# Kernel optimization log

Measured on AMD Instinct MI355X. Metric: run time of the kernel, lower is better.

## Reference

```python
import jax, jax.numpy as jnp
import numpy as np

DIM = 768
HEADS = 12
HEAD_DIM = DIM // HEADS
SCALE = HEAD_DIM ** (-0.5)
BATCH = 1
SEQ = 4096


def setup_inputs() -> dict:
    key = jax.random.key(0)
    ks = jax.random.split(key, 5)
    x = jax.random.normal(ks[0], (BATCH, SEQ, DIM), dtype=jnp.float32)
    # Linear params stored (in, out) for y = x @ W + b
    w_qkv = jax.random.normal(ks[1], (DIM, 3 * DIM), dtype=jnp.float32) * (DIM ** -0.5)
    b_qkv = jnp.zeros((3 * DIM,), dtype=jnp.float32)
    w_proj = jax.random.normal(ks[2], (DIM, DIM), dtype=jnp.float32) * (DIM ** -0.5)
    b_proj = jnp.zeros((DIM,), dtype=jnp.float32)
    return {"x": x, "w_qkv": w_qkv, "b_qkv": b_qkv, "w_proj": w_proj, "b_proj": b_proj}


def reference(x, w_qkv, b_qkv, w_proj, b_proj):
    B, S, _ = x.shape
    qkv = x @ w_qkv + b_qkv                              # [B,S,3*DIM]
    qkv = qkv.reshape(B, S, 3, HEADS, HEAD_DIM)
    q, k, v = qkv[:, :, 0], qkv[:, :, 1], qkv[:, :, 2]   # [B,S,H,D]
    # scaled dot-product attention, full score matrix as in the original
    attn = jnp.einsum("bqhd,bkhd->bhqk", q * SCALE, k)   # [B,H,S,S]
    attn = jax.nn.softmax(attn, axis=-1)
    out = jnp.einsum("bhqk,bkhd->bqhd", attn, v)         # [B,S,H,D]
    out = out.reshape(B, S, DIM)
    return out @ w_proj + b_proj
```

## Files before the change

### kernel.cpp

```cpp
#include <hip/hip_runtime.h>
#include <hip/hip_bf16.h>

#define SEQ   4096
#define DIM   768
#define HEADS 12
#define NQKV  2304
#define QSCALE 0.18033688011f

#if __has_builtin(__builtin_amdgcn_exp2f)
#define EXP2(x) __builtin_amdgcn_exp2f(x)
#else
#define EXP2(x) __expf((x) * 0.69314718056f)
#endif

typedef __bf16 bf16_t;
typedef bf16_t bf16x8 __attribute__((ext_vector_type(8)));
typedef float  f32x4  __attribute__((ext_vector_type(4)));
typedef float  f32x16 __attribute__((ext_vector_type(16)));
typedef unsigned short u16;
typedef unsigned int   u32;

static __device__ __forceinline__ float bf2f(u16 v) {
    union { float f; unsigned u; } x; x.u = ((unsigned)v) << 16; return x.f;
}
static __device__ __forceinline__ u16 f2bf(float f) {
    union { float f; unsigned u; } x; x.f = f;
    unsigned r = x.u + 0x7fff + ((x.u >> 16) & 1);
    return (u16)(r >> 16);
}
static __device__ __forceinline__ u32 fbits(float f) {
    union { float f; unsigned u; } x; x.f = f; return x.u;
}
static __device__ __forceinline__ void gload_lds16(const u16* g, u16* l) {
    __builtin_amdgcn_global_load_lds(
        (const __attribute__((address_space(1))) unsigned int*)g,
        (__attribute__((address_space(3))) unsigned int*)l, 16, 0, 0);
}

static __device__ __forceinline__ int detect_f32(const u32* __restrict__ x) {
    int lane = threadIdx.x & 63;
    int cnt = 0;
#pragma unroll
    for (int i = 0; i < 8; ++i) {
        u32 w = x[lane * 8 + i];
        cnt += (((w >> 7) & 0xFF) >= 0x8F) ? 1 : 0;
    }
#pragma unroll
    for (int m = 1; m < 64; m <<= 1) cnt += __shfl_xor(cnt, m);
    return cnt >= 64;
}

__global__ __launch_bounds__(256) void prep(
    const void* __restrict__ x, const void* __restrict__ wqkv,
    const void* __restrict__ bqkv, const void* __restrict__ wproj,
    const void* __restrict__ bproj,
    u16* __restrict__ cvt, u16* __restrict__ wqkvT, u16* __restrict__ wprojT)
{
    __shared__ u16 tile[64][65];
    const bool f32 = detect_f32((const u32*)x) != 0;
    const int b = blockIdx.x;
    const int t = threadIdx.x;

    if (b < 576) {
        const void* src; u16* dst; int K, N, tx, ty;
        if (b < 432) { src = wqkv; dst = wqkvT; K = DIM; N = NQKV; tx = b % 36; ty = b / 36; }
        else { int bb = b - 432; src = wproj; dst = wprojT; K = DIM; N = DIM; tx = bb % 12; ty = bb / 12; }
        const int k0 = ty * 64, n0 = tx * 64;
#pragma unroll
        for (int i = 0; i < 16; ++i) {
            int idx = i * 256 + t;
            int r = idx >> 6, c = idx & 63;
            size_t si = (size_t)(k0 + r) * N + n0 + c;
            tile[r][c] = f32 ? f2bf(((const float*)src)[si]) : ((const u16*)src)[si];
        }
        __syncthreads();
#pragma unroll
        for (int i = 0; i < 16; ++i) {
            int idx = i * 256 + t;
            int r = idx >> 6, c = idx & 63;
            dst[(size_t)(n0 + r) * K + k0 + c] = tile[c][r];
        }
    } else {
        const int SX = SEQ * DIM, e1 = SX + NQKV;
        const int n_cvt = e1 + DIM;
        for (int i = (b - 576) * 256 + t; i < n_cvt; i += 200 * 256) {
            const void* s; int off;
            if      (i < SX) { s = x; off = i; }
            else if (i < e1) { s = bqkv; off = i - SX; }
            else             { s = bproj; off = i - e1; }
            cvt[i] = f32 ? f2bf(((const float*)s)[off]) : ((const u16*)s)[off];
        }
    }
}

template<int MODE>
__global__ __launch_bounds__(256) void gemm128(
    const u16* __restrict__ A, const u16* __restrict__ BT, const u16* __restrict__ bias,
    u16* __restrict__ C0, float* __restrict__ Cf, u16* __restrict__ VT,
    const u32* __restrict__ xdet, int M, int N, int K)
{
    __shared__ u16 a_lds[128 * 32];
    __shared__ u16 b_lds[128 * 32];

    const int t    = threadIdx.x;
    const int w    = t >> 6;
    const int lane = t & 63;
    const int l15  = lane & 15;
    const int quad = lane >> 4;
    const int wm   = w >> 1, wn = w & 1;
    const int m0   = blockIdx.y * 128, n0 = blockIdx.x * 128;

    const int srow = w * 32 + (lane >> 2);
    const int kch  = (lane & 3) * 8;
    const u16* asrc = A  + (size_t)(m0 + srow) * K + kch;
    const u16* bsrc = BT + (size_t)(n0 + srow) * K + kch;
    u16* adst = a_lds + w * 32 * 32;
    u16* bdst = b_lds + w * 32 * 32;

    f32x4 acc[4][4] = {};

    for (int kt = 0; kt < K; kt += 32) {
        __syncthreads();
        gload_lds16(asrc,          adst);
        gload_lds16(asrc + 16 * K, adst + 16 * 32);
        gload_lds16(bsrc,          bdst);
        gload_lds16(bsrc + 16 * K, bdst + 16 * 32);
        asrc += 32; bsrc += 32;
        __syncthreads();

        const u16* ab = a_lds + (wm * 64 + l15) * 32 + quad * 8;
        const u16* bb = b_lds + (wn * 64 + l15) * 32 + quad * 8;
        bf16x8 af[4], bfr[4];
#pragma unroll
        for (int i = 0; i < 4; ++i) af[i]  = *(const bf16x8*)(ab + i * 16 * 32);
#pragma unroll
        for (int j = 0; j < 4; ++j) bfr[j] = *(const bf16x8*)(bb + j * 16 * 32);
#pragma unroll
        for (int i = 0; i < 4; ++i)
#pragma unroll
            for (int j = 0; j < 4; ++j)
                acc[i][j] = __builtin_amdgcn_mfma_f32_16x16x32_bf16(af[i], bfr[j], acc[i][j], 0, 0, 0);
    }

    if constexpr (MODE == 1) {
        if (n0 >= 1536) {
            __shared__ u16 t_lds[128 * 136];
#pragma unroll
            for (int i = 0; i < 4; ++i)
#pragma unroll
                for (int j = 0; j < 4; ++j)
#pragma unroll
                    for (int r = 0; r < 4; ++r) {
                        int ml = wm * 64 + i * 16 + quad * 4 + r;
                        int nl = wn * 64 + j * 16 + l15;
                        int mpl = (ml & ~15) | (ml & 3) |
                                  (((ml >> 2) & 1) << 3) | (((ml >> 3) & 1) << 2);
                        float v = acc[i][j][r] + bf2f(bias[n0 + nl]);
                        t_lds[nl * 136 + mpl] = f2bf(v);
                    }
            __syncthreads();
            const int rr = t >> 4;
            const int mo = (t & 15) * 8;
#pragma unroll
            for (int it = 0; it < 8; ++it) {
                int nl = rr + it * 16;
                *(bf16x8*)(VT + (size_t)(n0 - 1536 + nl) * SEQ + m0 + mo) =
                    *(const bf16x8*)(t_lds + nl * 136 + mo);
            }
            return;
        }
    }

    bool outf32 = false;
    if (MODE == 0) outf32 = detect_f32(xdet) != 0;
#pragma unroll
    for (int i = 0; i < 4; ++i)
#pragma unroll
        for (int j = 0; j < 4; ++j)
#pragma unroll
            for (int r = 0; r < 4; ++r) {
                int m = m0 + wm * 64 + i * 16 + quad * 4 + r;
                int n = n0 + wn * 64 + j * 16 + l15;
                float v = acc[i][j][r] + bf2f(bias[n]);
                if (MODE == 0) {
                    if (outf32) Cf[(size_t)m * N + n] = v;
                    else        C0[(size_t)m * N + n] = f2bf(v);
                } else {
                    float s = (n < 768) ? v * QSCALE : v;
                    C0[(size_t)m * 1536 + n] = f2bf(s);
                }
            }
}

__global__ __launch_bounds__(256, 3) void attn_kernel(
    const u16* __restrict__ qk, const u16* __restrict__ vt, u16* __restrict__ out)
{
    __shared__ u16 k_lds[3][64 * 64];
    __shared__ u16 v_lds[3][64 * 64];
    __shared__ float l_red[2][2][32];

    const int t    = threadIdx.x;
    const int w    = t >> 6;
    const int lane = t & 63;
    const int l31  = lane & 31;
    const int h    = lane >> 5;
    const int wq   = w & 1;
    const int wk   = w >> 1;

    const int lin     = blockIdx.x + (blockIdx.y << 6);
    const int logical = (lin & 7) * 96 + (lin >> 3);
    const int head    = logical >> 6;
    const int q0      = (logical & 63) * 64 + wq * 32;

    const u16* qrow = qk + (size_t)(q0 + l31) * 1536 + head * 64 + h * 8;
    bf16x8 qb[4];
#pragma unroll
    for (int s = 0; s < 4; ++s) qb[s] = *(const bf16x8*)(qrow + 16 * s);

    bf16x8 ones;
#pragma unroll
    for (int j = 0; j < 8; ++j) ones[j] = (bf16_t)1.0f;

    const f32x16 fz = {};

    const int srow = 8 * w + (lane >> 3);
    const int cs   = ((lane & 7) - srow) & 7;
    const u16* kst0 = qk + 768 + head * 64 + (size_t)srow * 1536 + cs * 8;
    const u16* kst1 = kst0 + (size_t)32 * 1536;
    const u16* vst0 = vt + (size_t)head * 64 * SEQ + (size_t)srow * SEQ + cs * 8;
    const u16* vst1 = vst0 + (size_t)32 * SEQ;
    const int woff = 8 * w * 64;

    const int krow = 32 * wk + l31;

    f32x16 o0 = {}, o1 = {}, lac = {};

    auto SK = [&](u16* kd) {
        gload_lds16(kst0, kd + woff);
        gload_lds16(kst1, kd + woff + 32 * 64);
        kst0 += (size_t)64 * 1536;
        kst1 += (size_t)64 * 1536;
    };
    auto SV = [&](u16* vd) {
        gload_lds16(vst0, vd + woff);
        gload_lds16(vst1, vd + woff + 32 * 64);
        vst0 += 64;
        vst1 += 64;
    };

    auto QK = [&](const u16* kb) -> f32x16 {
        const u16* kbase = kb + krow * 64;
        bf16x8 ka0 = *(const bf16x8*)(kbase + (((0 + h + krow) & 7) * 8));
        bf16x8 ka1 = *(const bf16x8*)(kbase + (((2 + h + krow) & 7) * 8));
        bf16x8 ka2 = *(const bf16x8*)(kbase + (((4 + h + krow) & 7) * 8));
        bf16x8 ka3 = *(const bf16x8*)(kbase + (((6 + h + krow) & 7) * 8));
        __builtin_amdgcn_s_setprio(1);
        f32x16 st = __builtin_amdgcn_mfma_f32_32x32x16_bf16(ka0, qb[0], fz, 0, 0, 0);
        st = __builtin_amdgcn_mfma_f32_32x32x16_bf16(ka1, qb[1], st, 0, 0, 0);
        st = __builtin_amdgcn_mfma_f32_32x32x16_bf16(ka2, qb[2], st, 0, 0, 0);
        st = __builtin_amdgcn_mfma_f32_32x32x16_bf16(ka3, qb[3], st, 0, 0, 0);
        __builtin_amdgcn_s_setprio(0);
        return st;
    };

    auto SMPV = [&](const f32x16& st, const u16* vb) {
        u32 q32[8];
#pragma unroll
        for (int i = 0; i < 8; ++i) {
            float pe = EXP2(st[2 * i]);
            float po = EXP2(st[2 * i + 1]);
            q32[i] = __builtin_amdgcn_perm(fbits(po), fbits(pe), 0x07060302u);
        }
        union { u32 u[4]; bf16x8 v; } pf0, pf1;
#pragma unroll
        for (int i = 0; i < 4; ++i) { pf0.u[i] = q32[i]; pf1.u[i] = q32[4 + i]; }
        __builtin_amdgcn_s_setprio(1);
#pragma unroll
        for (int s2 = 0; s2 < 2; ++s2) {
            const int c = 4 * wk + 2 * s2 + h;
            bf16x8 vb0 = *(const bf16x8*)(vb + l31 * 64 + (((c + l31) & 7) * 8));
            bf16x8 vb1 = *(const bf16x8*)(vb + (32 + l31) * 64 + (((c + 32 + l31) & 7) * 8));
            const bf16x8 pv = s2 ? pf1.v : pf0.v;
            o0  = __builtin_amdgcn_mfma_f32_32x32x16_bf16(pv, vb0, o0, 0, 0, 0);
            o1  = __builtin_amdgcn_mfma_f32_32x32x16_bf16(pv, vb1, o1, 0, 0, 0);
            lac = __builtin_amdgcn_mfma_f32_32x32x16_bf16(pv, ones, lac, 0, 0, 0);
        }
        __builtin_amdgcn_s_setprio(0);
    };

    u16 *kA = &k_lds[0][0], *kB = &k_lds[1][0], *kC = &k_lds[2][0];
    u16 *vA = &v_lds[0][0], *vB = &v_lds[1][0], *vC = &v_lds[2][0];

    SK(kA);
    SV(vA);
    SK(kB);
    asm volatile("s_waitcnt vmcnt(4)" ::: "memory");
    __builtin_amdgcn_s_barrier();
    f32x16 stA = QK(kA);
    SV(vB);
    f32x16 stB;

    for (int i = 0; i < 31; ++i) {
        SK(kC);
        asm volatile("s_waitcnt vmcnt(4)" ::: "memory");
        __builtin_amdgcn_s_barrier();
        stB = QK(kB);
        SMPV(stA, vA);
        SV(vC);
        { u16* tt = kA; kA = kB; kB = kC; kC = tt; }
        { u16* tt = vA; vA = vB; vB = vC; vC = tt; }
        SK(kC);
        asm volatile("s_waitcnt vmcnt(4)" ::: "memory");
        __builtin_amdgcn_s_barrier();
        stA = QK(kB);
        SMPV(stB, vA);
        SV(vC);
        { u16* tt = kA; kA = kB; kB = kC; kC = tt; }
        { u16* tt = vA; vA = vB; vB = vC; vC = tt; }
    }
    asm volatile("s_waitcnt vmcnt(2)" ::: "memory");
    __builtin_amdgcn_s_barrier();
    stB = QK(kB);
    SMPV(stA, vA);
    { u16* tt = kA; kA = kB; kB = kC; kC = tt; }
    { u16* tt = vA; vA = vB; vB = vC; vC = tt; }
    asm volatile("s_waitcnt vmcnt(0)" ::: "memory");
    __builtin_amdgcn_s_barrier();
    SMPV(stB, vA);
    __syncthreads();

    if (l31 == 0) {
#pragma unroll
        for (int r = 0; r < 16; ++r) {
            int row = (r & 3) + 8 * (r >> 2) + 4 * h;
            l_red[wq][wk][row] = lac[r];
        }
    }
    float* scr = (wq == 0) ? (float*)&k_lds[0][0] : (float*)&v_lds[0][0];
    if (wk == 1) {
#pragma unroll
        for (int r = 0; r < 16; ++r) {
            int row = (r & 3) + 8 * (r >> 2) + 4 * h;
            scr[row * 64 + l31]      = o0[r];
            scr[row * 64 + 32 + l31] = o1[r];
        }
    }
    __syncthreads();
    if (wk == 0) {
#pragma unroll
        for (int r = 0; r < 16; ++r) {
            int row = (r & 3) + 8 * (r >> 2) + 4 * h;
            float lt   = l_red[wq][0][row] + l_red[wq][1][row];
            float invl = 1.0f / lt;
            float s0 = o0[r] + scr[row * 64 + l31];
            float s1 = o1[r] + scr[row * 64 + 32 + l31];
            size_t gr = (size_t)(q0 + row) * 768 + head * 64;
            out[gr + l31]      = f2bf(s0 * invl);
            out[gr + 32 + l31] = f2bf(s1 * invl);
        }
    }
}

extern "C" void kernel_launch(void* const* d_in, const int* in_sizes, int n_in,
                              void* d_out, int out_size, void* d_ws, size_t ws_size,
                              hipStream_t stream) {
    const int SX = SEQ * DIM;

    u16* base   = (u16*)d_ws;
    u16* xb     = base;
    u16* bqkvb  = xb + SX;
    u16* bprojb = bqkvb + NQKV;
    u16* wqkvT  = bprojb + DIM;
    u16* wprojT = wqkvT + (size_t)NQKV * DIM;
    u16* qkb    = wprojT + (size_t)DIM * DIM;
    u16* vtb    = qkb + (size_t)SEQ * 1536;
    u16* attnb  = xb;

    prep<<<776, 256, 0, stream>>>(
        d_in[0], d_in[1], d_in[2], d_in[3], d_in[4], base, wqkvT, wprojT);
    gemm128<1><<<dim3(NQKV / 128, SEQ / 128), 256, 0, stream>>>(
        xb, wqkvT, bqkvb, qkb, nullptr, vtb, (const u32*)d_in[0],
        SEQ, NQKV, DIM);
    attn_kernel<<<dim3(SEQ / 64, HEADS), 256, 0, stream>>>(qkb, vtb, attnb);
    gemm128<0><<<dim3(DIM / 128, SEQ / 128), 256, 0, stream>>>(
        attnb, wprojT, bprojb, (u16*)d_out, (float*)d_out, nullptr,
        (const u32*)d_in[0], SEQ, DIM, DIM);
}
```

Measured before the change: 227.3 us.

## Triple-buffer GEMM LDS tiles to overlap global loads with MFMA compute

Replaces the single-buffered load-sync-compute loop in the 128x128 GEMM with a three-stage LDS ring. The prefetch runs two K-tiles ahead and is paced by vmcnt waits plus one barrier per iteration, so global-to-LDS latency can hide behind MFMA work. The transpose scratch buffer now shares the LDS union with the staging buffers. This costs more LDS per block, which may lower occupancy, and it depends on correct vmcnt accounting of the direct-to-LDS loads.

```diff
diff --git a/kernel.cpp b/kernel.cpp
--- a/kernel.cpp
+++ b/kernel.cpp
@@ -99,8 +99,10 @@
     u16* __restrict__ C0, float* __restrict__ Cf, u16* __restrict__ VT,
     const u32* __restrict__ xdet, int M, int N, int K)
 {
-    __shared__ u16 a_lds[128 * 32];
-    __shared__ u16 b_lds[128 * 32];
+    __shared__ union SharedLds {
+        struct { u16 a[3][128 * 32]; u16 b[3][128 * 32]; } s;
+        u16 t[128 * 136];
+    } lds;
 
     const int t    = threadIdx.x;
     const int w    = t >> 6;
@@ -114,22 +116,23 @@
     const int kch  = (lane & 3) * 8;
     const u16* asrc = A  + (size_t)(m0 + srow) * K + kch;
     const u16* bsrc = BT + (size_t)(n0 + srow) * K + kch;
-    u16* adst = a_lds + w * 32 * 32;
-    u16* bdst = b_lds + w * 32 * 32;
+    const int wst = w * 32 * 32;
 
     f32x4 acc[4][4] = {};
 
-    for (int kt = 0; kt < K; kt += 32) {
-        __syncthreads();
-        gload_lds16(asrc,          adst);
-        gload_lds16(asrc + 16 * K, adst + 16 * 32);
-        gload_lds16(bsrc,          bdst);
-        gload_lds16(bsrc + 16 * K, bdst + 16 * 32);
+    u16 *aA = lds.s.a[0], *aB = lds.s.a[1], *aC = lds.s.a[2];
+    u16 *bA = lds.s.b[0], *bB = lds.s.b[1], *bC = lds.s.b[2];
+
+    auto STAGE = [&](u16* ad, u16* bd) {
+        gload_lds16(asrc,          ad + wst);
+        gload_lds16(asrc + 16 * K, ad + wst + 16 * 32);
+        gload_lds16(bsrc,          bd + wst);
+        gload_lds16(bsrc + 16 * K, bd + wst + 16 * 32);
         asrc += 32; bsrc += 32;
-        __syncthreads();
-
-        const u16* ab = a_lds + (wm * 64 + l15) * 32 + quad * 8;
-        const u16* bb = b_lds + (wn * 64 + l15) * 32 + quad * 8;
+    };
+    auto COMPUTE = [&](const u16* ab_, const u16* bb_) {
+        const u16* ab = ab_ + (wm * 64 + l15) * 32 + quad * 8;
+        const u16* bb = bb_ + (wn * 64 + l15) * 32 + quad * 8;
         bf16x8 af[4], bfr[4];
 #pragma unroll
         for (int i = 0; i < 4; ++i) af[i]  = *(const bf16x8*)(ab + i * 16 * 32);
@@ -140,11 +143,31 @@
 #pragma unroll
             for (int j = 0; j < 4; ++j)
                 acc[i][j] = __builtin_amdgcn_mfma_f32_16x16x32_bf16(af[i], bfr[j], acc[i][j], 0, 0, 0);
-    }
+    };
+
+    const int NK = K >> 5;
+    STAGE(aA, bA);
+    STAGE(aB, bB);
+    for (int kt = 0; kt < NK - 2; ++kt) {
+        asm volatile("s_waitcnt vmcnt(4)" ::: "memory");
+        __builtin_amdgcn_s_barrier();
+        STAGE(aC, bC);
+        COMPUTE(aA, bA);
+        { u16* tt = aA; aA = aB; aB = aC; aC = tt; }
+        { u16* tt = bA; bA = bB; bB = bC; bC = tt; }
+    }
+    asm volatile("s_waitcnt vmcnt(4)" ::: "memory");
+    __builtin_amdgcn_s_barrier();
+    COMPUTE(aA, bA);
+    { u16* tt = aA; aA = aB; aB = aC; aC = tt; }
+    { u16* tt = bA; bA = bB; bB = bC; bC = tt; }
+    asm volatile("s_waitcnt vmcnt(0)" ::: "memory");
+    __builtin_amdgcn_s_barrier();
+    COMPUTE(aA, bA);
 
     if constexpr (MODE == 1) {
         if (n0 >= 1536) {
-            __shared__ u16 t_lds[128 * 136];
+            __syncthreads();
 #pragma unroll
             for (int i = 0; i < 4; ++i)
 #pragma unroll
@@ -156,7 +179,7 @@
                         int mpl = (ml & ~15) | (ml & 3) |
                                   (((ml >> 2) & 1) << 3) | (((ml >> 3) & 1) << 2);
                         float v = acc[i][j][r] + bf2f(bias[n0 + nl]);
-                        t_lds[nl * 136 + mpl] = f2bf(v);
+                        lds.t[nl * 136 + mpl] = f2bf(v);
                     }
             __syncthreads();
             const int rr = t >> 4;
@@ -165,7 +188,7 @@
             for (int it = 0; it < 8; ++it) {
                 int nl = rr + it * 16;
                 *(bf16x8*)(VT + (size_t)(n0 - 1536 + nl) * SEQ + m0 + mo) =
-                    *(const bf16x8*)(t_lds + nl * 136 + mo);
+                    *(const bf16x8*)(lds.t + nl * 136 + mo);
             }
             return;
         }
```

New measurement: 206.1 us. 1.1x faster.
